# Optimization experiments

Hardware: AMD Instinct MI355X
Metric: run time of the kernel (lower is better)

## Reference

```python
import jax, jax.numpy as jnp
import numpy as np

H = 2048          # hidden_size
NH = 16           # num_attention_heads
D = H // NH       # head dim = 128
FFN = 4 * H       # mlp hidden
EPS = 1e-5
NORM = float(np.sqrt(D))  # coeff=max(1,layer_number)=1 cancels in FusedScaleMaskSoftmax
NEG = -10000.0    # attention_mask_func fill value
L2EPS = 1e-12     # F.normalize eps


def layernorm(x, g, b):
    m = jnp.mean(x, axis=-1, keepdims=True)
    v = jnp.var(x, axis=-1, keepdims=True)
    return (x - m) * jax.lax.rsqrt(v + EPS) * g + b


def l2norm(x):
    n = jnp.sqrt(jnp.sum(x * x, axis=-1, keepdims=True))
    return x / jnp.maximum(n, L2EPS)


def mlp(x, w1, b1, w2, b2):
    # GPT MLP with skip_bias_add: returns (h@w2, bias)
    h = jax.nn.gelu(x @ w1 + b1, approximate=False)
    return h @ w2, b2


def setup_inputs():
    S, B, M = 2048, 2, 4096
    key = jax.random.key(0)
    ks = jax.random.split(key, 12)
    r = lambda i, shape: jax.random.normal(ks[i], shape, jnp.float32) * 0.02
    return {
        'x': jax.random.normal(ks[0], (S, B, H), jnp.float32),
        'past_hidden': jax.random.normal(ks[1], (M, B, H), jnp.float32),
        'mem_mask': jax.random.randint(ks[2], (B, 1, S, M), 0, 2) == 1,
        'ln1_g': jnp.ones((H,), jnp.float32), 'ln1_b': jnp.zeros((H,), jnp.float32),
        'ln2_g': jnp.ones((H,), jnp.float32), 'ln2_b': jnp.zeros((H,), jnp.float32),
        'ln3_g': jnp.ones((H,), jnp.float32), 'ln3_b': jnp.zeros((H,), jnp.float32),
        'mlp1_w1': r(3, (H, FFN)), 'mlp1_b1': jnp.zeros((FFN,), jnp.float32),
        'mlp1_w2': r(4, (FFN, H)), 'mlp1_b2': jnp.zeros((H,), jnp.float32),
        'mlp2_w1': r(5, (H, FFN)), 'mlp2_b1': jnp.zeros((FFN,), jnp.float32),
        'mlp2_w2': r(6, (FFN, H)), 'mlp2_b2': jnp.zeros((H,), jnp.float32),
        'wq': r(7, (H, H)), 'bq': jnp.zeros((H,), jnp.float32),
        'wkv': r(8, (H, 2 * H)), 'bkv': jnp.zeros((2 * H,), jnp.float32),
        'wd': r(9, (H, H)), 'bd': jnp.zeros((H,), jnp.float32),
    }


def reference(x, past_hidden, mem_mask, ln1_g, ln1_b, ln2_g, ln2_b, ln3_g, ln3_b,
              mlp1_w1, mlp1_b1, mlp1_w2, mlp1_b2, mlp2_w1, mlp2_b1, mlp2_w2, mlp2_b2,
              wq, bq, wkv, bkv, wd, bd):
    S, B, _ = x.shape
    M = past_hidden.shape[0]

    # mlp1 branch (output replaces x, residual is NOT added for mlp1 per source)
    o1, bias1 = mlp(layernorm(x, ln1_g, ln1_b), mlp1_w1, mlp1_b1, mlp1_w2, mlp1_b2)
    x = o1 + bias1

    # memory attention
    h = layernorm(x, ln2_g, ln2_b)
    q = l2norm((h @ wq + bq).reshape(S, B, NH, D))            # [S,B,NH,D]
    kv = (past_hidden @ wkv + bkv).reshape(M, B, NH, 2 * D)   # [M,B,NH,2D]
    k = l2norm(kv[..., :D])
    v = l2norm(kv[..., D:])
    scores = jnp.einsum('sbhd,mbhd->bhsm', q, k) / NORM       # [B,NH,S,M]
    scores = jnp.where(mem_mask, NEG, scores.astype(jnp.float32))
    probs = jax.nn.softmax(scores, axis=-1).astype(q.dtype)
    ctx = jnp.einsum('bhsm,mbhd->sbhd', probs, v).reshape(S, B, H)
    x = x + ctx @ wd + bd

    # mlp2 branch with residual
    o2, bias2 = mlp(layernorm(x, ln3_g, ln3_b), mlp2_w1, mlp2_b1, mlp2_w2, mlp2_b2)
    return x + o2 + bias2
```

## Files before the change

### kernel.cpp

```cpp
#include <hip/hip_runtime.h>


typedef unsigned short ushort_t;
typedef __attribute__((ext_vector_type(8))) short bf16x8;
typedef __attribute__((ext_vector_type(4))) float f32x4;

#define DEVI __device__ __forceinline__

DEVI ushort_t f2bf(float f) {
  unsigned int u = __builtin_bit_cast(unsigned int, f);
  u += 0x7FFFu + ((u >> 16) & 1u);
  return (ushort_t)(u >> 16);
}
DEVI float bf2f(ushort_t h) {
  unsigned int u = ((unsigned int)h) << 16;
  return __builtin_bit_cast(float, u);
}

DEVI void load_lds16(const void* g, void* l) {
  __builtin_amdgcn_global_load_lds(
      (__attribute__((address_space(1))) void*)(g),
      (__attribute__((address_space(3))) void*)(l), 16, 0, 0);
}

__global__ void detect_mask_k(const unsigned int* __restrict__ m, int* __restrict__ flag) {
  unsigned int v = m[threadIdx.x];
  unsigned long long ok = __ballot(v <= 1u);
  if (threadIdx.x == 0) *flag = (ok == ~0ull) ? 1 : 0;
}

__global__ __launch_bounds__(256)
void mask_pack_k(const void* __restrict__ maskp, const int* __restrict__ mtype,
                 unsigned long long* __restrict__ out, int nwords) {
  const int mint = *mtype;
  const int lane = threadIdx.x & 63;
  const int wglob = blockIdx.x * 4 + (threadIdx.x >> 6);
  const int nw = gridDim.x * 4;
  const unsigned char* m8 = (const unsigned char*)maskp;
  const int* m32 = (const int*)maskp;
  for (int i = wglob; i < nwords; i += nw) {
    const size_t e = (size_t)i * 64 + lane;
    const bool v = mint ? (m32[e] != 0) : (m8[e] != 0);
    unsigned long long bits = __ballot(v);
    if (lane == 0) out[i] = bits;
  }
}

__global__ __launch_bounds__(256)
void transpose_w(const float* __restrict__ in, ushort_t* __restrict__ out, int K, int N) {
  __shared__ float t[32][33];
  const int tx = threadIdx.x, ty = threadIdx.y;
  const int n0 = blockIdx.x * 32, k0 = blockIdx.y * 32;
#pragma unroll
  for (int i = 0; i < 4; ++i)
    t[ty + i * 8][tx] = in[(size_t)(k0 + ty + i * 8) * N + n0 + tx];
  __syncthreads();
#pragma unroll
  for (int i = 0; i < 4; ++i)
    out[(size_t)(n0 + ty + i * 8) * K + k0 + tx] = f2bf(t[tx][ty + i * 8]);
}

__global__ void f32_to_bf16_k(const float* __restrict__ in, ushort_t* __restrict__ out, int n4) {
  int i = blockIdx.x * blockDim.x + threadIdx.x;
  int stride = gridDim.x * blockDim.x;
  for (; i < n4; i += stride) {
    float4 v = ((const float4*)in)[i];
    ushort4 o;
    o.x = f2bf(v.x); o.y = f2bf(v.y); o.z = f2bf(v.z); o.w = f2bf(v.w);
    ((ushort4*)out)[i] = o;
  }
}

__global__ __launch_bounds__(256)
void ln_kernel(const float* __restrict__ in, const float* __restrict__ gam,
               const float* __restrict__ bet, ushort_t* __restrict__ out) {
  const int row = blockIdx.x;
  const float* p = in + (size_t)row * 2048;
  const int tid = threadIdx.x;
  float4 v0 = ((const float4*)p)[tid * 2];
  float4 v1 = ((const float4*)p)[tid * 2 + 1];
  float s = v0.x + v0.y + v0.z + v0.w + v1.x + v1.y + v1.z + v1.w;
  float q = v0.x * v0.x + v0.y * v0.y + v0.z * v0.z + v0.w * v0.w +
            v1.x * v1.x + v1.y * v1.y + v1.z * v1.z + v1.w * v1.w;
#pragma unroll
  for (int m = 1; m < 64; m <<= 1) { s += __shfl_xor(s, m); q += __shfl_xor(q, m); }
  __shared__ float red[8];
  const int w = tid >> 6;
  if ((tid & 63) == 0) { red[w] = s; red[4 + w] = q; }
  __syncthreads();
  s = red[0] + red[1] + red[2] + red[3];
  q = red[4] + red[5] + red[6] + red[7];
  const float mean = s * (1.f / 2048.f);
  const float var = q * (1.f / 2048.f) - mean * mean;
  const float rs = rsqrtf(var + 1e-5f);
  float4 g0 = ((const float4*)gam)[tid * 2], g1 = ((const float4*)gam)[tid * 2 + 1];
  float4 b0 = ((const float4*)bet)[tid * 2], b1 = ((const float4*)bet)[tid * 2 + 1];
  ushort4 o0, o1;
  o0.x = f2bf((v0.x - mean) * rs * g0.x + b0.x);
  o0.y = f2bf((v0.y - mean) * rs * g0.y + b0.y);
  o0.z = f2bf((v0.z - mean) * rs * g0.z + b0.z);
  o0.w = f2bf((v0.w - mean) * rs * g0.w + b0.w);
  o1.x = f2bf((v1.x - mean) * rs * g1.x + b1.x);
  o1.y = f2bf((v1.y - mean) * rs * g1.y + b1.y);
  o1.z = f2bf((v1.z - mean) * rs * g1.z + b1.z);
  o1.w = f2bf((v1.w - mean) * rs * g1.w + b1.w);
  ushort4* ob = (ushort4*)(out + (size_t)row * 2048);
  ob[tid * 2] = o0;
  ob[tid * 2 + 1] = o1;
}

__global__ __launch_bounds__(256)
void l2norm_seg(ushort_t* __restrict__ data, int nseg) {
  const int tid = threadIdx.x;
  const int w = tid >> 6, lane = tid & 63;
  const int seg = blockIdx.x * 4 + w;
  if (seg >= nseg) return;
  ushort_t* p = data + (size_t)seg * 128 + lane * 2;
  unsigned int pk = *(const unsigned int*)p;
  float a = bf2f((ushort_t)(pk & 0xFFFF));
  float b = bf2f((ushort_t)(pk >> 16));
  float ss = a * a + b * b;
#pragma unroll
  for (int m = 1; m < 64; m <<= 1) ss += __shfl_xor(ss, m);
  float inv = 1.f / fmaxf(sqrtf(ss), 1e-12f);
  unsigned int outp = (unsigned int)f2bf(a * inv) | ((unsigned int)f2bf(b * inv) << 16);
  *(unsigned int*)p = outp;
}

__global__ __launch_bounds__(256)
void vtrans_k(const ushort_t* __restrict__ kv, ushort_t* __restrict__ vt) {
  __shared__ ushort_t t[32][33];
  const int tx = threadIdx.x, ty = threadIdx.y;
  const int m0 = blockIdx.x * 32, d0 = blockIdx.y * 32, bh = blockIdx.z;
  const int b = bh >> 4, h = bh & 15;
#pragma unroll
  for (int i = 0; i < 4; ++i)
    t[ty + i * 8][tx] = kv[((size_t)(m0 + ty + i * 8) * 2 + b) * 4096 + h * 256 + 128 + d0 + tx];
  __syncthreads();
#pragma unroll
  for (int i = 0; i < 4; ++i)
    vt[((size_t)bh * 128 + d0 + ty + i * 8) * 4096 + m0 + tx] = t[tx][ty + i * 8];
}

template <int BM, int BN, int EPI>
__global__ __launch_bounds__(512, 2)
void gemm_t(const ushort_t* __restrict__ A, const ushort_t* __restrict__ Bt,
            const float* __restrict__ bias, const float* __restrict__ Xres,
            void* __restrict__ Out, int N, int K) {
  constexpr int WM = BM / 2, WN = BN / 4;
  constexpr int MREP = WM / 16, NREP = WN / 16;
  constexpr int AI = BM / 64, BI = BN / 64;
  __shared__ ushort_t lA[2][BM * 64];
  __shared__ ushort_t lB[2][BN * 64];

  const int tid = threadIdx.x;
  const int lane = tid & 63;
  const int w = tid >> 6;
  const int l15 = lane & 15, lhi = lane >> 4;
  const int wr = w >> 2, wc = w & 3;
  const int tm = blockIdx.x, tn = blockIdx.y;

  size_t aSrc[AI], bSrc[BI];
  int aDst[AI], bDst[BI];
#pragma unroll
  for (int i = 0; i < AI; ++i) {
    const int ch = (i * 8 + w) * 64 + lane;
    const int row = ch >> 3;
    const int colb = ((ch & 7) * 16) ^ ((row & 7) << 4);
    aSrc[i] = (size_t)(tm * BM + row) * K + (colb >> 1);
    aDst[i] = (i * 8 + w) * 1024;
  }
#pragma unroll
  for (int i = 0; i < BI; ++i) {
    const int ch = (i * 8 + w) * 64 + lane;
    const int row = ch >> 3;
    const int colb = ((ch & 7) * 16) ^ ((row & 7) << 4);
    bSrc[i] = (size_t)(tn * BN + row) * K + (colb >> 1);
    bDst[i] = (i * 8 + w) * 1024;
  }

  f32x4 acc[MREP][NREP] = {};

#pragma unroll
  for (int i = 0; i < AI; ++i) load_lds16(A + aSrc[i], (char*)lA[0] + aDst[i]);
#pragma unroll
  for (int i = 0; i < BI; ++i) load_lds16(Bt + bSrc[i], (char*)lB[0] + bDst[i]);
  __syncthreads();

  const int KT = K >> 6;
  int cur = 0;
  for (int kt = 0; kt < KT; ++kt) {
    if (kt + 1 < KT) {
      const int k0 = (kt + 1) * 64;
#pragma unroll
      for (int i = 0; i < AI; ++i)
        load_lds16(A + aSrc[i] + k0, (char*)lA[cur ^ 1] + aDst[i]);
#pragma unroll
      for (int i = 0; i < BI; ++i)
        load_lds16(Bt + bSrc[i] + k0, (char*)lB[cur ^ 1] + bDst[i]);
    }
#pragma unroll
    for (int kk = 0; kk < 2; ++kk) {
      const int kb = kk * 64 + lhi * 16;
      bf16x8 bfr[NREP];
#pragma unroll
      for (int nf = 0; nf < NREP; ++nf) {
        const int cb = wc * WN + nf * 16 + l15;
        bfr[nf] = *(const bf16x8*)((const char*)lB[cur] + cb * 128 + (kb ^ ((cb & 7) << 4)));
      }
#pragma unroll
      for (int mf = 0; mf < MREP; ++mf) {
        const int ra = wr * WM + mf * 16 + l15;
        bf16x8 af = *(const bf16x8*)((const char*)lA[cur] + ra * 128 + (kb ^ ((ra & 7) << 4)));
#pragma unroll
        for (int nf = 0; nf < NREP; ++nf)
          acc[mf][nf] = __builtin_amdgcn_mfma_f32_16x16x32_bf16(af, bfr[nf], acc[mf][nf], 0, 0, 0);
      }
    }
    __syncthreads();
    cur ^= 1;
  }

  const int row0 = tm * BM + wr * WM;
  const int col0 = tn * BN + wc * WN;
  float bj[NREP];
#pragma unroll
  for (int nf = 0; nf < NREP; ++nf) bj[nf] = bias[col0 + nf * 16 + l15];

#pragma unroll
  for (int mf = 0; mf < MREP; ++mf) {
#pragma unroll
    for (int nf = 0; nf < NREP; ++nf) {
      const int col = col0 + nf * 16 + l15;
#pragma unroll
      for (int r = 0; r < 4; ++r) {
        const int row = row0 + mf * 16 + lhi * 4 + r;
        const size_t idx = (size_t)row * N + col;
        float v = acc[mf][nf][r] + bj[nf];
        if constexpr (EPI == 0) {
          v = 0.5f * v * (1.f + erff(v * 0.70710678118654752f));
          ((ushort_t*)Out)[idx] = f2bf(v);
        } else if constexpr (EPI == 1) {
          ((ushort_t*)Out)[idx] = f2bf(v);
        } else if constexpr (EPI == 2) {
          ((float*)Out)[idx] = v;
        } else {
          ((float*)Out)[idx] = Xres[idx] + v;
        }
      }
    }
  }
}

__global__ __launch_bounds__(512, 4)
void attn_k(const ushort_t* __restrict__ Q, const ushort_t* __restrict__ KV,
            const ushort_t* __restrict__ VT,
            const unsigned long long* __restrict__ PM,
            ushort_t* __restrict__ CTX) {
  __shared__ ushort_t lk[2][64 * 128];
  __shared__ ushort_t lvt[2][128 * 64];
  __shared__ ushort_t lp[8][16 * 64];

  const int tid = threadIdx.x, lane = tid & 63, w = tid >> 6;
  const int l15 = lane & 15, lhi = lane >> 4;
  const int qt = blockIdx.x & 15, pair = blockIdx.x >> 4;
  const int b = pair >> 4, h = pair & 15;

  size_t kSrc[2], vSrc[2];
  int kDst[2], vDst[2];
#pragma unroll
  for (int i = 0; i < 2; ++i) {
    const int ch = (i * 8 + w) * 64 + lane;
    {
      const int row = ch >> 4;
      const int cb = ((ch & 15) * 16) ^ ((row & 7) << 4);
      kSrc[i] = ((size_t)row * 2 + b) * 4096 + h * 256 + (cb >> 1);
      kDst[i] = (i * 8 + w) * 1024;
    }
    {
      const int row = ch >> 3;
      const int cb = ((ch & 7) * 16) ^ ((row & 7) << 4);
      vSrc[i] = (size_t)pair * 128 * 4096 + (size_t)row * 4096 + (cb >> 1);
      vDst[i] = (i * 8 + w) * 1024;
    }
  }

  bf16x8 aq[4];
  {
    const ushort_t* qbase =
        Q + ((size_t)(qt * 128 + w * 16 + l15) * 2 + b) * 2048 + h * 128 + lhi * 8;
#pragma unroll
    for (int kk = 0; kk < 4; ++kk) aq[kk] = *(const bf16x8*)(qbase + kk * 32);
  }

  float l_acc[4] = {0.f, 0.f, 0.f, 0.f};
  f32x4 acc_o[8] = {};
  const float sscale = 0.088388347648318447f;
  const unsigned long long* mrow =
      PM + (size_t)(b * 2048 + qt * 128 + w * 16 + lhi * 4) * 64;
  const int l15p16 = l15 + 16;

#pragma unroll
  for (int i = 0; i < 2; ++i) {
    load_lds16(KV + kSrc[i], (char*)lk[0] + kDst[i]);
    load_lds16(VT + vSrc[i], (char*)lvt[0] + vDst[i]);
  }
  __syncthreads();

  int cur = 0;
  for (int t = 0; t < 64; ++t) {
    if (t < 63) {
      const size_t kAdd = (size_t)(t + 1) * 64 * 8192;
      const int vAdd = (t + 1) * 64;
#pragma unroll
      for (int i = 0; i < 2; ++i) {
        load_lds16(KV + kSrc[i] + kAdd, (char*)lk[cur ^ 1] + kDst[i]);
        load_lds16(VT + vSrc[i] + vAdd, (char*)lvt[cur ^ 1] + vDst[i]);
      }
    }
    unsigned long long mw[4];
#pragma unroll
    for (int r = 0; r < 4; ++r) mw[r] = mrow[r * 64 + t];

    f32x4 sa[4] = {};
#pragma unroll
    for (int kk = 0; kk < 4; ++kk) {
#pragma unroll
      for (int j = 0; j < 4; ++j) {
        const int krow = j * 16 + l15;
        const int bcb = (kk * 64 + lhi * 16) ^ ((krow & 7) << 4);
        bf16x8 bk = *(const bf16x8*)((const char*)lk[cur] + krow * 256 + bcb);
        sa[j] = __builtin_amdgcn_mfma_f32_16x16x32_bf16(aq[kk], bk, sa[j], 0, 0, 0);
      }
    }

#pragma unroll
    for (int r = 0; r < 4; ++r) {
      const unsigned int mlo = (unsigned int)mw[r];
      const unsigned int mhi = (unsigned int)(mw[r] >> 32);
#pragma unroll
      for (int j = 0; j < 4; ++j) {
        const unsigned int sel = (j < 2) ? mlo : mhi;
        const int sh = (j & 1) ? l15p16 : l15;
        const bool mk = (sel >> sh) & 1u;
        float tt = sa[j][r] * sscale;
        tt = mk ? -10000.f : tt;
        const float p = __expf(tt);
        sa[j][r] = p;
        l_acc[r] += p;
      }
    }

#pragma unroll
    for (int r = 0; r < 4; ++r) {
      unsigned int pk0, pk1;
      asm("v_cvt_pk_bf16_f32 %0, %1, %2" : "=v"(pk0) : "v"(sa[0][r]), "v"(sa[1][r]));
      asm("v_cvt_pk_bf16_f32 %0, %1, %2" : "=v"(pk1) : "v"(sa[2][r]), "v"(sa[3][r]));
      const int prow = lhi * 4 + r;
      char* base = (char*)lp[w] + prow * 128;
      const int swz = (prow & 7) << 4;
      *(ushort_t*)(base + ((l15 * 2) ^ swz)) = (ushort_t)pk0;
      *(ushort_t*)(base + (((16 + l15) * 2) ^ swz)) = (ushort_t)(pk0 >> 16);
      *(ushort_t*)(base + (((32 + l15) * 2) ^ swz)) = (ushort_t)pk1;
      *(ushort_t*)(base + (((48 + l15) * 2) ^ swz)) = (ushort_t)(pk1 >> 16);
    }

#pragma unroll
    for (int ks = 0; ks < 2; ++ks) {
      const int acb2 = (ks * 64 + lhi * 16) ^ ((l15 & 7) << 4);
      bf16x8 ap = *(const bf16x8*)((const char*)lp[w] + l15 * 128 + acb2);
#pragma unroll
      for (int d = 0; d < 8; ++d) {
        const int vrow = d * 16 + l15;
        const int vcb = (ks * 64 + lhi * 16) ^ ((vrow & 7) << 4);
        bf16x8 bv = *(const bf16x8*)((const char*)lvt[cur] + vrow * 128 + vcb);
        acc_o[d] = __builtin_amdgcn_mfma_f32_16x16x32_bf16(ap, bv, acc_o[d], 0, 0, 0);
      }
    }
    __syncthreads();
    cur ^= 1;
  }

#pragma unroll
  for (int ms = 1; ms < 16; ms <<= 1)
#pragma unroll
    for (int r = 0; r < 4; ++r) l_acc[r] += __shfl_xor(l_acc[r], ms);

#pragma unroll
  for (int r = 0; r < 4; ++r) {
    const float inv = 1.f / fmaxf(l_acc[r], 1e-20f);
    const size_t orow = ((size_t)(qt * 128 + w * 16 + lhi * 4 + r) * 2 + b) * 2048 + h * 128;
#pragma unroll
    for (int d = 0; d < 8; ++d)
      CTX[orow + d * 16 + l15] = f2bf(acc_o[d][r] * inv);
  }
}

extern "C" void kernel_launch(void* const* d_in, const int* in_sizes, int n_in,
                              void* d_out, int out_size, void* d_ws, size_t ws_size,
                              hipStream_t stream) {
  (void)in_sizes; (void)n_in; (void)out_size; (void)ws_size;
  const float* x    = (const float*)d_in[0];
  const float* ph   = (const float*)d_in[1];
  const void*  mask = d_in[2];
  const float* ln1g = (const float*)d_in[3];
  const float* ln1b = (const float*)d_in[4];
  const float* ln2g = (const float*)d_in[5];
  const float* ln2b = (const float*)d_in[6];
  const float* ln3g = (const float*)d_in[7];
  const float* ln3b = (const float*)d_in[8];
  const float* w1a  = (const float*)d_in[9];
  const float* b1a  = (const float*)d_in[10];
  const float* w2a  = (const float*)d_in[11];
  const float* b2a  = (const float*)d_in[12];
  const float* w1b  = (const float*)d_in[13];
  const float* b1b  = (const float*)d_in[14];
  const float* w2b  = (const float*)d_in[15];
  const float* b2b  = (const float*)d_in[16];
  const float* wq   = (const float*)d_in[17];
  const float* bq   = (const float*)d_in[18];
  const float* wkv  = (const float*)d_in[19];
  const float* bkv  = (const float*)d_in[20];
  const float* wd   = (const float*)d_in[21];
  const float* bd   = (const float*)d_in[22];

  char* ws = (char*)d_ws;
  int* flag = (int*)ws;
  size_t off = 256;
  auto alloc = [&](size_t bytes) {
    void* p = ws + off;
    off += (bytes + 255) & ~(size_t)255;
    return p;
  };
  ushort_t* WT1   = (ushort_t*)alloc(2048ull * 8192 * 2);
  ushort_t* WT2   = (ushort_t*)alloc(2048ull * 8192 * 2);
  ushort_t* WQT   = (ushort_t*)alloc(2048ull * 2048 * 2);
  ushort_t* WKVT  = (ushort_t*)alloc(2048ull * 4096 * 2);
  ushort_t* WDT   = (ushort_t*)alloc(2048ull * 2048 * 2);
  ushort_t* H1    = (ushort_t*)alloc(4096ull * 2048 * 2);
  ushort_t* GELU  = (ushort_t*)alloc(4096ull * 8192 * 2);
  float*    X     = (float*)alloc(4096ull * 2048 * 4);
  ushort_t* QRAW  = (ushort_t*)alloc(4096ull * 2048 * 2);
  ushort_t* PH16  = (ushort_t*)alloc(8192ull * 2048 * 2);
  ushort_t* KVRAW = (ushort_t*)alloc(8192ull * 4096 * 2);
  ushort_t* VT    = PH16;
  ushort_t* CTX   = WKVT;
  unsigned long long* PMASK = (unsigned long long*)GELU;

  const dim3 tb(32, 8);

  detect_mask_k<<<1, 64, 0, stream>>>((const unsigned int*)mask, flag);

  transpose_w<<<dim3(256, 64), tb, 0, stream>>>(w1a, WT1, 2048, 8192);
  transpose_w<<<dim3(64, 256), tb, 0, stream>>>(w2a, WT2, 8192, 2048);
  transpose_w<<<dim3(64, 64), tb, 0, stream>>>(wq, WQT, 2048, 2048);
  transpose_w<<<dim3(128, 64), tb, 0, stream>>>(wkv, WKVT, 2048, 4096);
  transpose_w<<<dim3(64, 64), tb, 0, stream>>>(wd, WDT, 2048, 2048);

  ln_kernel<<<4096, 256, 0, stream>>>(x, ln1g, ln1b, H1);
  gemm_t<256, 256, 0><<<dim3(16, 32), 512, 0, stream>>>(H1, WT1, b1a, nullptr, GELU, 8192, 2048);
  gemm_t<128, 256, 2><<<dim3(32, 8), 512, 0, stream>>>(GELU, WT2, b2a, nullptr, X, 2048, 8192);

  mask_pack_k<<<1024, 256, 0, stream>>>(mask, flag, PMASK, 262144);

  ln_kernel<<<4096, 256, 0, stream>>>(X, ln2g, ln2b, H1);
  gemm_t<128, 256, 1><<<dim3(32, 8), 512, 0, stream>>>(H1, WQT, bq, nullptr, QRAW, 2048, 2048);
  l2norm_seg<<<65536 / 4, 256, 0, stream>>>(QRAW, 65536);
  f32_to_bf16_k<<<2048, 256, 0, stream>>>(ph, PH16, 8192 * 2048 / 4);
  gemm_t<256, 256, 1><<<dim3(32, 16), 512, 0, stream>>>(PH16, WKVT, bkv, nullptr, KVRAW, 4096, 2048);
  l2norm_seg<<<262144 / 4, 256, 0, stream>>>(KVRAW, 262144);
  vtrans_k<<<dim3(128, 4, 32), tb, 0, stream>>>(KVRAW, VT);
  attn_k<<<512, 512, 0, stream>>>(QRAW, KVRAW, VT, PMASK, CTX);
  gemm_t<128, 256, 3><<<dim3(32, 8), 512, 0, stream>>>(CTX, WDT, bd, X, X, 2048, 2048);

  ln_kernel<<<4096, 256, 0, stream>>>(X, ln3g, ln3b, H1);
  transpose_w<<<dim3(256, 64), tb, 0, stream>>>(w1b, WT1, 2048, 8192);
  transpose_w<<<dim3(64, 256), tb, 0, stream>>>(w2b, WT2, 8192, 2048);
  gemm_t<256, 256, 0><<<dim3(16, 32), 512, 0, stream>>>(H1, WT1, b1b, nullptr, GELU, 8192, 2048);
  gemm_t<128, 256, 3><<<dim3(32, 8), 512, 0, stream>>>(GELU, WT2, b2b, X, d_out, 2048, 8192);
}
```

Before: 1.516 ms.

## Deepen GEMM LDS prefetch with explicit vmcnt waits and XCD-aware tile swizzle

```diff
diff --git a/kernel.cpp b/kernel.cpp
--- a/kernel.cpp
+++ b/kernel.cpp
@@ -21,6 +21,18 @@
   __builtin_amdgcn_global_load_lds(
       (__attribute__((address_space(1))) void*)(g),
       (__attribute__((address_space(3))) void*)(l), 16, 0, 0);
+}
+
+DEVI void block_sync() {
+  asm volatile("" ::: "memory");
+  __builtin_amdgcn_s_barrier();
+  __builtin_amdgcn_sched_barrier(0);
+}
+
+template <int N> DEVI void waitcnt_vm() {
+  if constexpr (N == 8) asm volatile("s_waitcnt vmcnt(8)" ::: "memory");
+  else if constexpr (N == 6) asm volatile("s_waitcnt vmcnt(6)" ::: "memory");
+  else asm volatile("s_waitcnt vmcnt(0)" ::: "memory");
 }
 
 __global__ void detect_mask_k(const unsigned int* __restrict__ m, int* __restrict__ flag) {
@@ -144,12 +156,13 @@
 
 template <int BM, int BN, int EPI>
 __global__ __launch_bounds__(512, 2)
-void gemm_t(const ushort_t* __restrict__ A, const ushort_t* __restrict__ Bt,
+void gemm_p(const ushort_t* __restrict__ A, const ushort_t* __restrict__ Bt,
             const float* __restrict__ bias, const float* __restrict__ Xres,
-            void* __restrict__ Out, int N, int K) {
+            void* __restrict__ Out, int N, int K, int GM) {
   constexpr int WM = BM / 2, WN = BN / 4;
   constexpr int MREP = WM / 16, NREP = WN / 16;
-  constexpr int AI = BM / 64, BI = BN / 64;
+  constexpr int ACH = BM / 64, BCH = BN / 64;
+  constexpr int LPT = ACH + BCH;
   __shared__ ushort_t lA[2][BM * 64];
   __shared__ ushort_t lB[2][BN * 64];
 
@@ -158,67 +171,79 @@
   const int w = tid >> 6;
   const int l15 = lane & 15, lhi = lane >> 4;
   const int wr = w >> 2, wc = w & 3;
-  const int tm = blockIdx.x, tn = blockIdx.y;
-
-  size_t aSrc[AI], bSrc[BI];
-  int aDst[AI], bDst[BI];
-#pragma unroll
-  for (int i = 0; i < AI; ++i) {
-    const int ch = (i * 8 + w) * 64 + lane;
+
+  const int nwg = gridDim.x;
+  const int cpx = nwg >> 3;
+  const int swz = (blockIdx.x & 7) * cpx + (blockIdx.x >> 3);
+  const int tm = swz % GM, tn = swz / GM;
+
+  size_t aSrc[ACH], bSrc[BCH];
+#pragma unroll
+  for (int i = 0; i < ACH; ++i) {
+    const int ch = i * 512 + tid;
     const int row = ch >> 3;
     const int colb = ((ch & 7) * 16) ^ ((row & 7) << 4);
     aSrc[i] = (size_t)(tm * BM + row) * K + (colb >> 1);
-    aDst[i] = (i * 8 + w) * 1024;
-  }
-#pragma unroll
-  for (int i = 0; i < BI; ++i) {
-    const int ch = (i * 8 + w) * 64 + lane;
+  }
+#pragma unroll
+  for (int i = 0; i < BCH; ++i) {
+    const int ch = i * 512 + tid;
     const int row = ch >> 3;
     const int colb = ((ch & 7) * 16) ^ ((row & 7) << 4);
     bSrc[i] = (size_t)(tn * BN + row) * K + (colb >> 1);
-    bDst[i] = (i * 8 + w) * 1024;
-  }
+  }
+
+  auto stage = [&](int kt, int buf) {
+    const int k0 = kt << 6;
+#pragma unroll
+    for (int i = 0; i < ACH; ++i)
+      load_lds16(A + aSrc[i] + k0, (char*)lA[buf] + (i * 512 + tid) * 16);
+#pragma unroll
+    for (int i = 0; i < BCH; ++i)
+      load_lds16(Bt + bSrc[i] + k0, (char*)lB[buf] + (i * 512 + tid) * 16);
+  };
 
   f32x4 acc[MREP][NREP] = {};
 
-#pragma unroll
-  for (int i = 0; i < AI; ++i) load_lds16(A + aSrc[i], (char*)lA[0] + aDst[i]);
-#pragma unroll
-  for (int i = 0; i < BI; ++i) load_lds16(Bt + bSrc[i], (char*)lB[0] + bDst[i]);
-  __syncthreads();
-
   const int KT = K >> 6;
-  int cur = 0;
+  stage(0, 0);
+  stage(1, 1);
+  waitcnt_vm<LPT>();
+  block_sync();
+
   for (int kt = 0; kt < KT; ++kt) {
-    if (kt + 1 < KT) {
-      const int k0 = (kt + 1) * 64;
-#pragma unroll
-      for (int i = 0; i < AI; ++i)
-        load_lds16(A + aSrc[i] + k0, (char*)lA[cur ^ 1] + aDst[i]);
-#pragma unroll
-      for (int i = 0; i < BI; ++i)
-        load_lds16(Bt + bSrc[i] + k0, (char*)lB[cur ^ 1] + bDst[i]);
-    }
-#pragma unroll
-    for (int kk = 0; kk < 2; ++kk) {
-      const int kb = kk * 64 + lhi * 16;
-      bf16x8 bfr[NREP];
+    const int cur = kt & 1;
+    const char* bufA = (const char*)lA[cur];
+    const char* bufB = (const char*)lB[cur];
+    bf16x8 bfr[NREP][2];
+#pragma unroll
+    for (int nf = 0; nf < NREP; ++nf) {
+      const int rb = wc * WN + nf * 16 + l15;
+      const int sw = (rb & 7) << 4;
+#pragma unroll
+      for (int kk = 0; kk < 2; ++kk)
+        bfr[nf][kk] = *(const bf16x8*)(bufB + rb * 128 + ((kk * 64 + lhi * 16) ^ sw));
+    }
+#pragma unroll
+    for (int mf = 0; mf < MREP; ++mf) {
+      const int ra = wr * WM + mf * 16 + l15;
+      const int sw = (ra & 7) << 4;
+      bf16x8 af0 = *(const bf16x8*)(bufA + ra * 128 + ((lhi * 16) ^ sw));
+      bf16x8 af1 = *(const bf16x8*)(bufA + ra * 128 + ((64 + lhi * 16) ^ sw));
 #pragma unroll
       for (int nf = 0; nf < NREP; ++nf) {
-        const int cb = wc * WN + nf * 16 + l15;
-        bfr[nf] = *(const bf16x8*)((const char*)lB[cur] + cb * 128 + (kb ^ ((cb & 7) << 4)));
+        acc[mf][nf] = __builtin_amdgcn_mfma_f32_16x16x32_bf16(af0, bfr[nf][0], acc[mf][nf], 0, 0, 0);
+        acc[mf][nf] = __builtin_amdgcn_mfma_f32_16x16x32_bf16(af1, bfr[nf][1], acc[mf][nf], 0, 0, 0);
       }
-#pragma unroll
-      for (int mf = 0; mf < MREP; ++mf) {
-        const int ra = wr * WM + mf * 16 + l15;
-        bf16x8 af = *(const bf16x8*)((const char*)lA[cur] + ra * 128 + (kb ^ ((ra & 7) << 4)));
-#pragma unroll
-        for (int nf = 0; nf < NREP; ++nf)
-          acc[mf][nf] = __builtin_amdgcn_mfma_f32_16x16x32_bf16(af, bfr[nf], acc[mf][nf], 0, 0, 0);
-      }
-    }
-    __syncthreads();
-    cur ^= 1;
+    }
+    block_sync();
+    if (kt + 2 < KT) {
+      stage(kt + 2, cur);
+      waitcnt_vm<LPT>();
+    } else {
+      waitcnt_vm<0>();
+    }
+    block_sync();
   }
 
   const int row0 = tm * BM + wr * WM;
@@ -458,24 +483,24 @@
   transpose_w<<<dim3(64, 64), tb, 0, stream>>>(wd, WDT, 2048, 2048);
 
   ln_kernel<<<4096, 256, 0, stream>>>(x, ln1g, ln1b, H1);
-  gemm_t<256, 256, 0><<<dim3(16, 32), 512, 0, stream>>>(H1, WT1, b1a, nullptr, GELU, 8192, 2048);
-  gemm_t<128, 256, 2><<<dim3(32, 8), 512, 0, stream>>>(GELU, WT2, b2a, nullptr, X, 2048, 8192);
+  gemm_p<256, 256, 0><<<512, 512, 0, stream>>>(H1, WT1, b1a, nullptr, GELU, 8192, 2048, 16);
+  gemm_p<128, 256, 2><<<256, 512, 0, stream>>>(GELU, WT2, b2a, nullptr, X, 2048, 8192, 32);
 
   mask_pack_k<<<1024, 256, 0, stream>>>(mask, flag, PMASK, 262144);
 
   ln_kernel<<<4096, 256, 0, stream>>>(X, ln2g, ln2b, H1);
-  gemm_t<128, 256, 1><<<dim3(32, 8), 512, 0, stream>>>(H1, WQT, bq, nullptr, QRAW, 2048, 2048);
+  gemm_p<128, 256, 1><<<256, 512, 0, stream>>>(H1, WQT, bq, nullptr, QRAW, 2048, 2048, 32);
   l2norm_seg<<<65536 / 4, 256, 0, stream>>>(QRAW, 65536);
   f32_to_bf16_k<<<2048, 256, 0, stream>>>(ph, PH16, 8192 * 2048 / 4);
-  gemm_t<256, 256, 1><<<dim3(32, 16), 512, 0, stream>>>(PH16, WKVT, bkv, nullptr, KVRAW, 4096, 2048);
+  gemm_p<256, 256, 1><<<512, 512, 0, stream>>>(PH16, WKVT, bkv, nullptr, KVRAW, 4096, 2048, 32);
   l2norm_seg<<<262144 / 4, 256, 0, stream>>>(KVRAW, 262144);
   vtrans_k<<<dim3(128, 4, 32), tb, 0, stream>>>(KVRAW, VT);
   attn_k<<<512, 512, 0, stream>>>(QRAW, KVRAW, VT, PMASK, CTX);
-  gemm_t<128, 256, 3><<<dim3(32, 8), 512, 0, stream>>>(CTX, WDT, bd, X, X, 2048, 2048);
+  gemm_p<128, 256, 3><<<256, 512, 0, stream>>>(CTX, WDT, bd, X, X, 2048, 2048, 32);
 
   ln_kernel<<<4096, 256, 0, stream>>>(X, ln3g, ln3b, H1);
   transpose_w<<<dim3(256, 64), tb, 0, stream>>>(w1b, WT1, 2048, 8192);
   transpose_w<<<dim3(64, 256), tb, 0, stream>>>(w2b, WT2, 8192, 2048);
-  gemm_t<256, 256, 0><<<dim3(16, 32), 512, 0, stream>>>(H1, WT1, b1b, nullptr, GELU, 8192, 2048);
-  gemm_t<128, 256, 3><<<dim3(32, 8), 512, 0, stream>>>(GELU, WT2, b2b, X, d_out, 2048, 8192);
-}
+  gemm_p<256, 256, 0><<<512, 512, 0, stream>>>(H1, WT1, b1b, nullptr, GELU, 8192, 2048, 16);
+  gemm_p<128, 256, 3><<<256, 512, 0, stream>>>(GELU, WT2, b2b, X, d_out, 2048, 8192, 32);
+}
```

Measured after the change: 1.550 ms. +2.2%, slower.
